# Kernel optimization log

Hardware: AMD Instinct MI355X
Metric: run time of the kernel (lower is better)

The kernel has to match this reference:

```python
import jax, jax.numpy as jnp
import numpy as np

EMBED_DIM = 1024
HEAD_DIM = 64


def setup_inputs() -> dict:
    key = jax.random.key(0)
    ks = jax.random.split(key, 7)
    s_in = EMBED_DIM ** -0.5  # torch Linear default init scale
    x = jax.random.normal(ks[0], (4, 4096, EMBED_DIM), dtype=jnp.float32)
    Wk = jax.random.uniform(ks[1], (HEAD_DIM, EMBED_DIM), jnp.float32, -s_in, s_in)
    bk = jax.random.uniform(ks[2], (HEAD_DIM,), jnp.float32, -s_in, s_in)
    Wq = jax.random.uniform(ks[3], (HEAD_DIM, EMBED_DIM), jnp.float32, -s_in, s_in)
    bq = jax.random.uniform(ks[4], (HEAD_DIM,), jnp.float32, -s_in, s_in)
    Wv = jax.random.uniform(ks[5], (HEAD_DIM, EMBED_DIM), jnp.float32, -s_in, s_in)
    bv = jax.random.uniform(ks[6], (HEAD_DIM,), jnp.float32, -s_in, s_in)
    return {"x": x, "Wq": Wq, "bq": bq, "Wk": Wk, "bk": bk, "Wv": Wv, "bv": bv}


def reference(x, Wq, bq, Wk, bk, Wv, bv):
    # torch Linear: y = x @ W.T + b
    q = jnp.einsum('btc,dc->btd', x, Wq) + bq  # [B,T,D]
    k = jnp.einsum('btc,dc->btd', x, Wk) + bk
    v = jnp.einsum('btc,dc->btd', x, Wv) + bv
    scale = HEAD_DIM ** -0.5
    # NOTE: original divides by scale (multiplies by sqrt(head_dim)) -- faithful
    scores = jnp.einsum('btd,bsd->bts', q, k) / scale  # [B,T,T]
    attn_weights = jax.nn.softmax(scores, axis=-1)
    return jnp.einsum('bts,bsd->btd', attn_weights, v)
```

## Files before the change

### kernel.cpp

```cpp
#include <hip/hip_runtime.h>

#define BATCH 4
#define SEQ   4096
#define CDIM  1024
#define DDIM  64
#define NROW  (BATCH * SEQ)
#define SP    72
#define SPA   70

typedef _Float16 f16;
typedef _Float16 f16x8 __attribute__((ext_vector_type(8)));
typedef _Float16 f16x4 __attribute__((ext_vector_type(4)));
typedef __fp16   h16x2 __attribute__((ext_vector_type(2)));
typedef float    f32x4 __attribute__((ext_vector_type(4)));

#define MFMA16(a, b, c) __builtin_amdgcn_mfma_f32_16x16x32_f16((a), (b), (c), 0, 0, 0)

#define QSCALE 11.5415603f

__device__ inline f16x8 cvt8(f32x4 a, f32x4 b) {
  h16x2 p0 = __builtin_amdgcn_cvt_pkrtz(a[0], a[1]);
  h16x2 p1 = __builtin_amdgcn_cvt_pkrtz(a[2], a[3]);
  h16x2 p2 = __builtin_amdgcn_cvt_pkrtz(b[0], b[1]);
  h16x2 p3 = __builtin_amdgcn_cvt_pkrtz(b[2], b[3]);
  f16x8 r;
  r[0] = p0[0]; r[1] = p0[1]; r[2] = p1[0]; r[3] = p1[1];
  r[4] = p2[0]; r[5] = p2[1]; r[6] = p3[0]; r[7] = p3[1];
  return r;
}

__device__ inline f16x4 cvt4(float a, float b, float c, float d) {
  h16x2 lo = __builtin_amdgcn_cvt_pkrtz(a, b);
  h16x2 hi = __builtin_amdgcn_cvt_pkrtz(c, d);
  f16x4 r;
  r[0] = lo[0]; r[1] = lo[1]; r[2] = hi[0]; r[3] = hi[1];
  return r;
}

__global__ __launch_bounds__(256) void proj_kernel(const float* __restrict__ x,
                                                   const float* __restrict__ Wq,
                                                   const float* __restrict__ Wk,
                                                   const float* __restrict__ Wv,
                                                   const float* __restrict__ bq,
                                                   const float* __restrict__ bk,
                                                   const float* __restrict__ bv,
                                                   f16* __restrict__ qs,
                                                   f16* __restrict__ ks,
                                                   f16* __restrict__ vT) {
  __shared__ __attribute__((aligned(16))) f16 lw[192][SP];
  const int tid = threadIdx.x;
  const int lane = tid & 63, w = tid >> 6;
  const int n = lane & 15, quad = lane >> 4;
  const int rowbase = blockIdx.x * 64 + w * 16;
  const int srow = tid >> 2;
  const int scol = (tid & 3) * 8;

  const float* Wm[3] = {Wq, Wk, Wv};

  f32x4 acc[3][4];
#pragma unroll
  for (int m_ = 0; m_ < 3; ++m_)
#pragma unroll
    for (int t_ = 0; t_ < 4; ++t_) acc[m_][t_] = (f32x4){0.f, 0.f, 0.f, 0.f};

  const float* xrow = x + (size_t)(rowbase + n) * CDIM + quad * 8;

  f32x4 wr[3][2];
  f32x4 xr0, xr1;
#define WLOAD(KC)                                                          \
  {                                                                        \
    _Pragma("unroll") for (int i = 0; i < 3; ++i) {                        \
      const float* p = Wm[i] + (size_t)srow * CDIM + (KC) + scol;          \
      wr[i][0] = *(const f32x4*)p;                                         \
      wr[i][1] = *(const f32x4*)(p + 4);                                   \
    }                                                                      \
  }
#define XLOAD(KC)                          \
  {                                        \
    xr0 = *(const f32x4*)(xrow + (KC));    \
    xr1 = *(const f32x4*)(xrow + (KC) + 4); \
  }

  WLOAD(0);
  XLOAD(0);
  for (int kc = 0; kc < CDIM; kc += 32) {
#pragma unroll
    for (int i = 0; i < 3; ++i) *(f16x8*)&lw[i * 64 + srow][scol] = cvt8(wr[i][0], wr[i][1]);
    __syncthreads();
    if (kc + 32 < CDIM) WLOAD(kc + 32);
    const f16x8 a = cvt8(xr0, xr1);
    if (kc + 32 < CDIM) XLOAD(kc + 32);
#pragma unroll
    for (int mat = 0; mat < 3; ++mat)
#pragma unroll
      for (int tile = 0; tile < 4; ++tile) {
        const f16x8 bf = *(const f16x8*)&lw[mat * 64 + tile * 16 + n][quad * 8];
        acc[mat][tile] = MFMA16(a, bf, acc[mat][tile]);
      }
    __syncthreads();
  }

  const float* bias_p[3] = {bq, bk, bv};
#pragma unroll
  for (int mat = 0; mat < 3; ++mat)
#pragma unroll
    for (int tile = 0; tile < 4; ++tile) {
      const int d = tile * 16 + n;
      const float bias = bias_p[mat][d];
      const int row0 = rowbase + quad * 4;
      f32x4 a = acc[mat][tile];
      if (mat == 0) {
#pragma unroll
        for (int r = 0; r < 4; ++r)
          qs[(size_t)(row0 + r) * DDIM + d] = (f16)((a[r] + bias) * QSCALE);
      } else if (mat == 1) {
#pragma unroll
        for (int r = 0; r < 4; ++r)
          ks[(size_t)(row0 + r) * DDIM + d] = (f16)(a[r] + bias);
      } else {
        const int bb = row0 >> 12;
        const int t = row0 & (SEQ - 1);
        f16x4 pk = cvt4(a[0] + bias, a[1] + bias, a[2] + bias, a[3] + bias);
        *(f16x4*)(vT + (size_t)(bb * 64 + d) * SEQ + t) = pk;
      }
    }
}

template <int NSPLIT>
__global__ __launch_bounds__(256, 4) void attn_kernel(const f16* __restrict__ qs,
                                                      const f16* __restrict__ ks,
                                                      const f16* __restrict__ vT,
                                                      float* __restrict__ outp,
                                                      float* __restrict__ pm,
                                                      float* __restrict__ pl) {
  __shared__ __attribute__((aligned(16))) f16 lk[64][SPA];
  __shared__ __attribute__((aligned(16))) f16 lv[64][SPA];
  __shared__ __attribute__((aligned(16))) f16 pb[4][32][SPA];
  const int tid = threadIdx.x, lane = tid & 63, w = tid >> 6;
  const int n = lane & 15, quad = lane >> 4;
  const int split = blockIdx.x % NSPLIT;
  const int rowblk = blockIdx.x / NSPLIT;
  const int row0 = rowblk * 128 + w * 32;
  const int bb = row0 >> 12;
  const int kbase = split * (SEQ / NSPLIT);
  const int NC = SEQ / NSPLIT / 64;

  const f16* kb = ks + (size_t)bb * SEQ * DDIM;
  const f16* vb = vT + (size_t)bb * DDIM * SEQ;

  const int srow = tid >> 2;
  const int scol = (tid & 3) * 16;
  const f16* kgp = kb + (size_t)(kbase + srow) * DDIM + scol;
  const f16* vgp = vb + (size_t)srow * SEQ + kbase + scol;

  f16x8 qf[2][2];
#pragma unroll
  for (int g = 0; g < 2; ++g)
#pragma unroll
    for (int h = 0; h < 2; ++h)
      qf[g][h] = *(const f16x8*)(qs + (size_t)(row0 + g * 16 + n) * DDIM + h * 32 + quad * 8);

  f32x4 acc[2][4];
  float m[2] = {-1e30f, -1e30f}, ll[2] = {0.f, 0.f};
#pragma unroll
  for (int g = 0; g < 2; ++g)
#pragma unroll
    for (int t = 0; t < 4; ++t) acc[g][t] = (f32x4){0.f, 0.f, 0.f, 0.f};

  f16x8 kr0, kr1, vr0, vr1;
  auto gload = [&](int c) {
    const f16* kp = kgp + (size_t)c * 64 * DDIM;
    kr0 = *(const f16x8*)kp;
    kr1 = *(const f16x8*)(kp + 8);
    const f16* vp = vgp + c * 64;
    vr0 = *(const f16x8*)vp;
    vr1 = *(const f16x8*)(vp + 8);
  };

  gload(0);
  for (int c = 0; c < NC; ++c) {
    *(f16x8*)&lk[srow][scol] = kr0;
    *(f16x8*)&lk[srow][scol + 8] = kr1;
    *(f16x8*)&lv[srow][scol] = vr0;
    *(f16x8*)&lv[srow][scol + 8] = vr1;
    __syncthreads();
    if (c + 1 < NC) gload(c + 1);

    f32x4 s[2][4];
#pragma unroll
    for (int st = 0; st < 4; ++st) {
      const f16x8 klo = *(const f16x8*)&lk[st * 16 + n][quad * 8];
      const f16x8 khi = *(const f16x8*)&lk[st * 16 + n][32 + quad * 8];
#pragma unroll
      for (int g = 0; g < 2; ++g) {
        f32x4 z = (f32x4){0.f, 0.f, 0.f, 0.f};
        z = MFMA16(klo, qf[g][0], z);
        s[g][st] = MFMA16(khi, qf[g][1], z);
      }
    }

#pragma unroll
    for (int g = 0; g < 2; ++g) {
      f32x4 mx;
#pragma unroll
      for (int r = 0; r < 4; ++r)
        mx[r] = fmaxf(fmaxf(s[g][0][r], s[g][1][r]), fmaxf(s[g][2][r], s[g][3][r]));
      float mloc = fmaxf(fmaxf(mx[0], mx[1]), fmaxf(mx[2], mx[3]));
      mloc = fmaxf(mloc, __shfl_xor(mloc, 16));
      mloc = fmaxf(mloc, __shfl_xor(mloc, 32));
      const float mnew = fmaxf(m[g], mloc);
      const float alpha = __builtin_amdgcn_exp2f(m[g] - mnew);
      m[g] = mnew;
      float psum = 0.f;
#pragma unroll
      for (int st = 0; st < 4; ++st) {
        f32x4 p;
#pragma unroll
        for (int r = 0; r < 4; ++r) p[r] = __builtin_amdgcn_exp2f(s[g][st][r] - mnew);
        psum += (p[0] + p[1]) + (p[2] + p[3]);
        *(f16x4*)&pb[w][g * 16 + n][st * 16 + quad * 4] = cvt4(p[0], p[1], p[2], p[3]);
      }
      ll[g] = ll[g] * alpha + psum;
#pragma unroll
      for (int t = 0; t < 4; ++t) acc[g][t] *= alpha;
    }
    __builtin_amdgcn_wave_barrier();

#pragma unroll
    for (int g = 0; g < 2; ++g) {
      const f16x8 pa0 = *(const f16x8*)&pb[w][g * 16 + n][quad * 8];
      const f16x8 pa1 = *(const f16x8*)&pb[w][g * 16 + n][32 + quad * 8];
#pragma unroll
      for (int t = 0; t < 4; ++t) {
        const f16x8 vlo = *(const f16x8*)&lv[t * 16 + n][quad * 8];
        const f16x8 vhi = *(const f16x8*)&lv[t * 16 + n][32 + quad * 8];
        acc[g][t] = MFMA16(vlo, pa0, acc[g][t]);
        acc[g][t] = MFMA16(vhi, pa1, acc[g][t]);
      }
    }
    __syncthreads();
  }

  float lred[2];
#pragma unroll
  for (int g = 0; g < 2; ++g) {
    float l = ll[g];
    l += __shfl_xor(l, 16);
    l += __shfl_xor(l, 32);
    lred[g] = l;
  }

  if (NSPLIT == 1) {
#pragma unroll
    for (int g = 0; g < 2; ++g) {
      const float inv = 1.0f / lred[g];
      const int q = row0 + g * 16 + n;
#pragma unroll
      for (int t = 0; t < 4; ++t) {
        f32x4 o = acc[g][t];
#pragma unroll
        for (int r = 0; r < 4; ++r) o[r] *= inv;
        *(f32x4*)(outp + (size_t)q * DDIM + t * 16 + quad * 4) = o;
      }
    }
  } else {
#pragma unroll
    for (int g = 0; g < 2; ++g) {
      const int q = row0 + g * 16 + n;
#pragma unroll
      for (int t = 0; t < 4; ++t)
        *(f32x4*)(outp + ((size_t)split * NROW + q) * DDIM + t * 16 + quad * 4) = acc[g][t];
      if (quad == 0) {
        pm[split * NROW + q] = m[g];
        pl[split * NROW + q] = lred[g];
      }
    }
  }
}

template <int NSPLIT>
__global__ __launch_bounds__(256) void combine_kernel(const float* __restrict__ pacc,
                                                      const float* __restrict__ pm,
                                                      const float* __restrict__ pl,
                                                      float* __restrict__ out) {
  const int idx = blockIdx.x * 256 + threadIdx.x;
  const int row = idx >> 4;
  const int c = (idx & 15) * 4;
  float mm = pm[row];
#pragma unroll
  for (int s = 1; s < NSPLIT; ++s) mm = fmaxf(mm, pm[s * NROW + row]);
  float L = 0.f;
  f32x4 o = (f32x4){0.f, 0.f, 0.f, 0.f};
#pragma unroll
  for (int s = 0; s < NSPLIT; ++s) {
    const float e = __builtin_amdgcn_exp2f(pm[s * NROW + row] - mm);
    L += pl[s * NROW + row] * e;
    const f32x4 a = *(const f32x4*)(pacc + ((size_t)s * NROW + row) * DDIM + c);
#pragma unroll
    for (int j = 0; j < 4; ++j) o[j] += a[j] * e;
  }
  const float inv = 1.0f / L;
#pragma unroll
  for (int j = 0; j < 4; ++j) o[j] *= inv;
  *(f32x4*)(out + (size_t)row * DDIM + c) = o;
}

extern "C" void kernel_launch(void* const* d_in, const int* in_sizes, int n_in,
                              void* d_out, int out_size, void* d_ws, size_t ws_size,
                              hipStream_t stream) {
  const float* x  = (const float*)d_in[0];
  const float* Wq = (const float*)d_in[1];
  const float* bq = (const float*)d_in[2];
  const float* Wk = (const float*)d_in[3];
  const float* bk = (const float*)d_in[4];
  const float* Wv = (const float*)d_in[5];
  const float* bv = (const float*)d_in[6];
  float* out = (float*)d_out;

  f16* qs = (f16*)d_ws;
  f16* ks = qs + (size_t)NROW * DDIM;
  f16* vT = ks + (size_t)NROW * DDIM;
  char* endf16 = (char*)(vT + (size_t)NROW * DDIM);

  float* pacc = (float*)endf16;
  const size_t base = (size_t)(endf16 - (char*)d_ws);
  const size_t need8 = base + (size_t)8 * NROW * (DDIM + 2) * 4;
  const size_t need4 = base + (size_t)4 * NROW * (DDIM + 2) * 4;

  proj_kernel<<<dim3(256), dim3(256), 0, stream>>>(x, Wq, Wk, Wv, bq, bk, bv, qs, ks, vT);

  if (ws_size >= need8) {
    float* pm = pacc + (size_t)8 * NROW * DDIM;
    float* pl = pm + (size_t)8 * NROW;
    attn_kernel<8><<<dim3(128 * 8), dim3(256), 0, stream>>>(qs, ks, vT, pacc, pm, pl);
    combine_kernel<8><<<dim3(NROW * 16 / 256), dim3(256), 0, stream>>>(pacc, pm, pl, out);
  } else if (ws_size >= need4) {
    float* pm = pacc + (size_t)4 * NROW * DDIM;
    float* pl = pm + (size_t)4 * NROW;
    attn_kernel<4><<<dim3(128 * 4), dim3(256), 0, stream>>>(qs, ks, vT, pacc, pm, pl);
    combine_kernel<4><<<dim3(NROW * 16 / 256), dim3(256), 0, stream>>>(pacc, pm, pl, out);
  } else {
    attn_kernel<1><<<dim3(128), dim3(256), 0, stream>>>(qs, ks, vT, out, nullptr, nullptr);
  }
}
```

Baseline: 168.8 us.

## Pre-convert weights, split-K projection, register P for PV MFMA, fp16 partials

Adds a prep kernel that converts Wq/Wk/Wv to fp16 once, so the projection kernel loads half-width weights and skips the per-tile conversion. The projection kernel now uses 32-row blocks with a two-way K split across wave pairs, reduced through shared memory, which doubles the grid. The attention kernel stops staging P in LDS and feeds the softmax fragments straight from registers into 16x16x16 MFMAs, and it stores split partials as fp16 to halve combine traffic. The costs are an extra launch, a second MFMA shape, and lower precision in the partial accumulators.

```diff
diff --git a/kernel.cpp b/kernel.cpp
--- a/kernel.cpp
+++ b/kernel.cpp
@@ -5,8 +5,9 @@
 #define CDIM  1024
 #define DDIM  64
 #define NROW  (BATCH * SEQ)
-#define SP    72
+#define SPW   40
 #define SPA   70
+#define NSPL  8
 
 typedef _Float16 f16;
 typedef _Float16 f16x8 __attribute__((ext_vector_type(8)));
@@ -14,7 +15,8 @@
 typedef __fp16   h16x2 __attribute__((ext_vector_type(2)));
 typedef float    f32x4 __attribute__((ext_vector_type(4)));
 
-#define MFMA16(a, b, c) __builtin_amdgcn_mfma_f32_16x16x32_f16((a), (b), (c), 0, 0, 0)
+#define MFMA32(a, b, c) __builtin_amdgcn_mfma_f32_16x16x32_f16((a), (b), (c), 0, 0, 0)
+#define MFMA16(a, b, c) __builtin_amdgcn_mfma_f32_16x16x16f16((a), (b), (c), 0, 0, 0)
 
 #define QSCALE 11.5415603f
 
@@ -37,25 +39,48 @@
   return r;
 }
 
-__global__ __launch_bounds__(256) void proj_kernel(const float* __restrict__ x,
-                                                   const float* __restrict__ Wq,
-                                                   const float* __restrict__ Wk,
-                                                   const float* __restrict__ Wv,
-                                                   const float* __restrict__ bq,
-                                                   const float* __restrict__ bk,
-                                                   const float* __restrict__ bv,
-                                                   f16* __restrict__ qs,
-                                                   f16* __restrict__ ks,
-                                                   f16* __restrict__ vT) {
-  __shared__ __attribute__((aligned(16))) f16 lw[192][SP];
+__global__ __launch_bounds__(256) void prep_w_kernel(const float* __restrict__ Wq,
+                                                     const float* __restrict__ Wk,
+                                                     const float* __restrict__ Wv,
+                                                     f16* __restrict__ wf) {
+  const int i = (blockIdx.x * 256 + threadIdx.x) * 4;
+  f32x4 a = *(const f32x4*)(Wq + i);
+  f32x4 b = *(const f32x4*)(Wk + i);
+  f32x4 c = *(const f32x4*)(Wv + i);
+  *(f16x4*)(wf + i)          = cvt4(a[0], a[1], a[2], a[3]);
+  *(f16x4*)(wf + 65536 + i)  = cvt4(b[0], b[1], b[2], b[3]);
+  *(f16x4*)(wf + 131072 + i) = cvt4(c[0], c[1], c[2], c[3]);
+}
+
+__global__ __launch_bounds__(256, 2) void proj_kernel(const float* __restrict__ x,
+                                                      const f16* __restrict__ wf,
+                                                      const float* __restrict__ bq,
+                                                      const float* __restrict__ bk,
+                                                      const float* __restrict__ bv,
+                                                      f16* __restrict__ qs,
+                                                      f16* __restrict__ ks,
+                                                      f16* __restrict__ vT) {
+  __shared__ __attribute__((aligned(16))) char smem[2 * 192 * SPW * 2];
+  f16(*lw)[192][SPW] = (f16(*)[192][SPW])smem;
+  f32x4(*comb)[64][12] = (f32x4(*)[64][12])smem;
+
   const int tid = threadIdx.x;
   const int lane = tid & 63, w = tid >> 6;
   const int n = lane & 15, quad = lane >> 4;
-  const int rowbase = blockIdx.x * 64 + w * 16;
-  const int srow = tid >> 2;
-  const int scol = (tid & 3) * 8;
-
-  const float* Wm[3] = {Wq, Wk, Wv};
+  const int h = w >> 1;
+  const int rw = w & 1;
+  const int rowbase = blockIdx.x * 32;
+  const int row0w = rowbase + rw * 16;
+
+  int sh[6], srow[6], sc8[6];
+#pragma unroll
+  for (int i = 0; i < 6; ++i) {
+    const int id = tid + 256 * i;
+    sh[i] = id / 768;
+    const int rem = id - sh[i] * 768;
+    srow[i] = rem >> 2;
+    sc8[i] = (rem & 3) * 8;
+  }
 
   f32x4 acc[3][4];
 #pragma unroll
@@ -63,42 +88,56 @@
 #pragma unroll
     for (int t_ = 0; t_ < 4; ++t_) acc[m_][t_] = (f32x4){0.f, 0.f, 0.f, 0.f};
 
-  const float* xrow = x + (size_t)(rowbase + n) * CDIM + quad * 8;
-
-  f32x4 wr[3][2];
+  const float* xrow = x + (size_t)(row0w + n) * CDIM + h * 512 + quad * 8;
+
+  f16x8 wreg[6];
   f32x4 xr0, xr1;
-#define WLOAD(KC)                                                          \
-  {                                                                        \
-    _Pragma("unroll") for (int i = 0; i < 3; ++i) {                        \
-      const float* p = Wm[i] + (size_t)srow * CDIM + (KC) + scol;          \
-      wr[i][0] = *(const f32x4*)p;                                         \
-      wr[i][1] = *(const f32x4*)(p + 4);                                   \
-    }                                                                      \
-  }
-#define XLOAD(KC)                          \
-  {                                        \
-    xr0 = *(const f32x4*)(xrow + (KC));    \
+#define WLOADP(KC)                                                                     \
+  {                                                                                    \
+    _Pragma("unroll") for (int i = 0; i < 6; ++i)                                      \
+        wreg[i] = *(const f16x8*)(wf + (size_t)srow[i] * CDIM + sh[i] * 512 + (KC) + sc8[i]); \
+  }
+#define XLOADP(KC)                          \
+  {                                         \
+    xr0 = *(const f32x4*)(xrow + (KC));     \
     xr1 = *(const f32x4*)(xrow + (KC) + 4); \
   }
 
-  WLOAD(0);
-  XLOAD(0);
-  for (int kc = 0; kc < CDIM; kc += 32) {
-#pragma unroll
-    for (int i = 0; i < 3; ++i) *(f16x8*)&lw[i * 64 + srow][scol] = cvt8(wr[i][0], wr[i][1]);
+  WLOADP(0);
+  XLOADP(0);
+  for (int kc = 0; kc < 512; kc += 32) {
+#pragma unroll
+    for (int i = 0; i < 6; ++i) *(f16x8*)&lw[sh[i]][srow[i]][sc8[i]] = wreg[i];
     __syncthreads();
-    if (kc + 32 < CDIM) WLOAD(kc + 32);
+    if (kc + 32 < 512) WLOADP(kc + 32);
     const f16x8 a = cvt8(xr0, xr1);
-    if (kc + 32 < CDIM) XLOAD(kc + 32);
+    if (kc + 32 < 512) XLOADP(kc + 32);
 #pragma unroll
     for (int mat = 0; mat < 3; ++mat)
 #pragma unroll
       for (int tile = 0; tile < 4; ++tile) {
-        const f16x8 bf = *(const f16x8*)&lw[mat * 64 + tile * 16 + n][quad * 8];
-        acc[mat][tile] = MFMA16(a, bf, acc[mat][tile]);
+        const f16x8 bf = *(const f16x8*)&lw[h][mat * 64 + tile * 16 + n][quad * 8];
+        acc[mat][tile] = MFMA32(a, bf, acc[mat][tile]);
       }
     __syncthreads();
   }
+
+  if (h == 1) {
+#pragma unroll
+    for (int m_ = 0; m_ < 3; ++m_)
+#pragma unroll
+      for (int t_ = 0; t_ < 4; ++t_) comb[rw][lane][m_ * 4 + t_] = acc[m_][t_];
+  }
+  __syncthreads();
+  if (h == 1) return;
+#pragma unroll
+  for (int m_ = 0; m_ < 3; ++m_)
+#pragma unroll
+    for (int t_ = 0; t_ < 4; ++t_) {
+      const f32x4 o = comb[rw][lane][m_ * 4 + t_];
+#pragma unroll
+      for (int r = 0; r < 4; ++r) acc[m_][t_][r] += o[r];
+    }
 
   const float* bias_p[3] = {bq, bk, bv};
 #pragma unroll
@@ -107,21 +146,21 @@
     for (int tile = 0; tile < 4; ++tile) {
       const int d = tile * 16 + n;
       const float bias = bias_p[mat][d];
-      const int row0 = rowbase + quad * 4;
+      const int r0 = row0w + quad * 4;
       f32x4 a = acc[mat][tile];
       if (mat == 0) {
 #pragma unroll
         for (int r = 0; r < 4; ++r)
-          qs[(size_t)(row0 + r) * DDIM + d] = (f16)((a[r] + bias) * QSCALE);
+          qs[(size_t)(r0 + r) * DDIM + d] = (f16)((a[r] + bias) * QSCALE);
       } else if (mat == 1) {
 #pragma unroll
         for (int r = 0; r < 4; ++r)
-          ks[(size_t)(row0 + r) * DDIM + d] = (f16)(a[r] + bias);
+          ks[(size_t)(r0 + r) * DDIM + d] = (f16)(a[r] + bias);
       } else {
-        const int bb = row0 >> 12;
-        const int t = row0 & (SEQ - 1);
-        f16x4 pk = cvt4(a[0] + bias, a[1] + bias, a[2] + bias, a[3] + bias);
-        *(f16x4*)(vT + (size_t)(bb * 64 + d) * SEQ + t) = pk;
+        const int bb = r0 >> 12;
+        const int t = r0 & (SEQ - 1);
+        *(f16x4*)(vT + (size_t)(bb * 64 + d) * SEQ + t) =
+            cvt4(a[0] + bias, a[1] + bias, a[2] + bias, a[3] + bias);
       }
     }
 }
@@ -131,11 +170,11 @@
                                                       const f16* __restrict__ ks,
                                                       const f16* __restrict__ vT,
                                                       float* __restrict__ outp,
+                                                      f16* __restrict__ pacc,
                                                       float* __restrict__ pm,
                                                       float* __restrict__ pl) {
   __shared__ __attribute__((aligned(16))) f16 lk[64][SPA];
   __shared__ __attribute__((aligned(16))) f16 lv[64][SPA];
-  __shared__ __attribute__((aligned(16))) f16 pb[4][32][SPA];
   const int tid = threadIdx.x, lane = tid & 63, w = tid >> 6;
   const int n = lane & 15, quad = lane >> 4;
   const int split = blockIdx.x % NSPLIT;
@@ -157,8 +196,8 @@
 #pragma unroll
   for (int g = 0; g < 2; ++g)
 #pragma unroll
-    for (int h = 0; h < 2; ++h)
-      qf[g][h] = *(const f16x8*)(qs + (size_t)(row0 + g * 16 + n) * DDIM + h * 32 + quad * 8);
+    for (int hh = 0; hh < 2; ++hh)
+      qf[g][hh] = *(const f16x8*)(qs + (size_t)(row0 + g * 16 + n) * DDIM + hh * 32 + quad * 8);
 
   f32x4 acc[2][4];
   float m[2] = {-1e30f, -1e30f}, ll[2] = {0.f, 0.f};
@@ -194,11 +233,12 @@
 #pragma unroll
       for (int g = 0; g < 2; ++g) {
         f32x4 z = (f32x4){0.f, 0.f, 0.f, 0.f};
-        z = MFMA16(klo, qf[g][0], z);
-        s[g][st] = MFMA16(khi, qf[g][1], z);
-      }
-    }
-
+        z = MFMA32(klo, qf[g][0], z);
+        s[g][st] = MFMA32(khi, qf[g][1], z);
+      }
+    }
+
+    f16x4 pq[2][4];
 #pragma unroll
     for (int g = 0; g < 2; ++g) {
       f32x4 mx;
@@ -218,26 +258,21 @@
 #pragma unroll
         for (int r = 0; r < 4; ++r) p[r] = __builtin_amdgcn_exp2f(s[g][st][r] - mnew);
         psum += (p[0] + p[1]) + (p[2] + p[3]);
-        *(f16x4*)&pb[w][g * 16 + n][st * 16 + quad * 4] = cvt4(p[0], p[1], p[2], p[3]);
+        pq[g][st] = cvt4(p[0], p[1], p[2], p[3]);
       }
       ll[g] = ll[g] * alpha + psum;
 #pragma unroll
       for (int t = 0; t < 4; ++t) acc[g][t] *= alpha;
     }
-    __builtin_amdgcn_wave_barrier();
-
-#pragma unroll
-    for (int g = 0; g < 2; ++g) {
-      const f16x8 pa0 = *(const f16x8*)&pb[w][g * 16 + n][quad * 8];
-      const f16x8 pa1 = *(const f16x8*)&pb[w][g * 16 + n][32 + quad * 8];
-#pragma unroll
-      for (int t = 0; t < 4; ++t) {
-        const f16x8 vlo = *(const f16x8*)&lv[t * 16 + n][quad * 8];
-        const f16x8 vhi = *(const f16x8*)&lv[t * 16 + n][32 + quad * 8];
-        acc[g][t] = MFMA16(vlo, pa0, acc[g][t]);
-        acc[g][t] = MFMA16(vhi, pa1, acc[g][t]);
-      }
-    }
+
+#pragma unroll
+    for (int t = 0; t < 4; ++t)
+#pragma unroll
+      for (int st = 0; st < 4; ++st) {
+        const f16x4 va = *(const f16x4*)&lv[t * 16 + n][st * 16 + quad * 4];
+        acc[0][t] = MFMA16(va, pq[0][st], acc[0][t]);
+        acc[1][t] = MFMA16(va, pq[1][st], acc[1][t]);
+      }
     __syncthreads();
   }
 
@@ -269,7 +304,8 @@
       const int q = row0 + g * 16 + n;
 #pragma unroll
       for (int t = 0; t < 4; ++t)
-        *(f32x4*)(outp + ((size_t)split * NROW + q) * DDIM + t * 16 + quad * 4) = acc[g][t];
+        *(f16x4*)(pacc + ((size_t)split * NROW + q) * DDIM + t * 16 + quad * 4) =
+            cvt4(acc[g][t][0], acc[g][t][1], acc[g][t][2], acc[g][t][3]);
       if (quad == 0) {
         pm[split * NROW + q] = m[g];
         pl[split * NROW + q] = lred[g];
@@ -279,7 +315,7 @@
 }
 
 template <int NSPLIT>
-__global__ __launch_bounds__(256) void combine_kernel(const float* __restrict__ pacc,
+__global__ __launch_bounds__(256) void combine_kernel(const f16* __restrict__ pacc,
                                                       const float* __restrict__ pm,
                                                       const float* __restrict__ pl,
                                                       float* __restrict__ out) {
@@ -295,9 +331,9 @@
   for (int s = 0; s < NSPLIT; ++s) {
     const float e = __builtin_amdgcn_exp2f(pm[s * NROW + row] - mm);
     L += pl[s * NROW + row] * e;
-    const f32x4 a = *(const f32x4*)(pacc + ((size_t)s * NROW + row) * DDIM + c);
-#pragma unroll
-    for (int j = 0; j < 4; ++j) o[j] += a[j] * e;
+    const f16x4 a = *(const f16x4*)(pacc + ((size_t)s * NROW + row) * DDIM + c);
+#pragma unroll
+    for (int j = 0; j < 4; ++j) o[j] += (float)a[j] * e;
   }
   const float inv = 1.0f / L;
 #pragma unroll
@@ -317,29 +353,22 @@
   const float* bv = (const float*)d_in[6];
   float* out = (float*)d_out;
 
-  f16* qs = (f16*)d_ws;
+  f16* wf = (f16*)d_ws;
+  f16* qs = wf + 3 * 65536;
   f16* ks = qs + (size_t)NROW * DDIM;
   f16* vT = ks + (size_t)NROW * DDIM;
-  char* endf16 = (char*)(vT + (size_t)NROW * DDIM);
-
-  float* pacc = (float*)endf16;
-  const size_t base = (size_t)(endf16 - (char*)d_ws);
-  const size_t need8 = base + (size_t)8 * NROW * (DDIM + 2) * 4;
-  const size_t need4 = base + (size_t)4 * NROW * (DDIM + 2) * 4;
-
-  proj_kernel<<<dim3(256), dim3(256), 0, stream>>>(x, Wq, Wk, Wv, bq, bk, bv, qs, ks, vT);
-
-  if (ws_size >= need8) {
-    float* pm = pacc + (size_t)8 * NROW * DDIM;
-    float* pl = pm + (size_t)8 * NROW;
-    attn_kernel<8><<<dim3(128 * 8), dim3(256), 0, stream>>>(qs, ks, vT, pacc, pm, pl);
-    combine_kernel<8><<<dim3(NROW * 16 / 256), dim3(256), 0, stream>>>(pacc, pm, pl, out);
-  } else if (ws_size >= need4) {
-    float* pm = pacc + (size_t)4 * NROW * DDIM;
-    float* pl = pm + (size_t)4 * NROW;
-    attn_kernel<4><<<dim3(128 * 4), dim3(256), 0, stream>>>(qs, ks, vT, pacc, pm, pl);
-    combine_kernel<4><<<dim3(NROW * 16 / 256), dim3(256), 0, stream>>>(pacc, pm, pl, out);
+  f16* pacc = vT + (size_t)NROW * DDIM;
+  float* pm = (float*)(pacc + (size_t)NSPL * NROW * DDIM);
+  float* pl = pm + (size_t)NSPL * NROW;
+  const size_t need = (size_t)((char*)(pl + (size_t)NSPL * NROW) - (char*)d_ws);
+
+  prep_w_kernel<<<dim3(64), dim3(256), 0, stream>>>(Wq, Wk, Wv, wf);
+  proj_kernel<<<dim3(512), dim3(256), 0, stream>>>(x, wf, bq, bk, bv, qs, ks, vT);
+
+  if (ws_size >= need) {
+    attn_kernel<NSPL><<<dim3(128 * NSPL), dim3(256), 0, stream>>>(qs, ks, vT, nullptr, pacc, pm, pl);
+    combine_kernel<NSPL><<<dim3(NROW * 16 / 256), dim3(256), 0, stream>>>(pacc, pm, pl, out);
   } else {
-    attn_kernel<1><<<dim3(128), dim3(256), 0, stream>>>(qs, ks, vT, out, nullptr, nullptr);
-  }
-}
+    attn_kernel<1><<<dim3(128), dim3(256), 0, stream>>>(qs, ks, vT, out, nullptr, nullptr, nullptr);
+  }
+}
```

Result: faster. 164.5 us (-2.5%).
